# Kernel tuning notes

Hardware: AMD Instinct MI355X
Metric: run time of the kernel (lower is better)

Reference implementation:

```python
import jax, jax.numpy as jnp
import numpy as np

N_NODES = 100000
N_EDGES = 1600000
N_KEEP = 1280000  # int(N_EDGES * (1 - thr_a)), thr_a = 0.2
F_IN = 128
F_OUT = 128


def setup_inputs() -> dict:
    key = jax.random.key(0)
    ks = jax.random.split(key, 7)
    x = jax.random.normal(ks[0], (N_NODES, F_IN), dtype=jnp.float32)
    W = jax.random.normal(ks[1], (F_OUT, F_IN), dtype=jnp.float32) * (1.0 / np.sqrt(F_IN))
    bias = jax.random.normal(ks[2], (F_OUT,), dtype=jnp.float32)
    edge_src = jax.random.randint(ks[3], (N_EDGES,), 0, N_NODES, dtype=jnp.int32)
    edge_dst = jax.random.randint(ks[4], (N_EDGES,), 0, N_NODES, dtype=jnp.int32)
    edge_weight = jax.random.uniform(ks[5], (N_EDGES,), dtype=jnp.float32)
    idx_keep = jax.random.randint(ks[6], (N_KEEP,), 0, N_EDGES, dtype=jnp.int32)
    return {"x": x, "W": W, "bias": bias, "edge_src": edge_src,
            "edge_dst": edge_dst, "edge_weight": edge_weight, "idx_keep": idx_keep}


def reference(x, W, bias, edge_src, edge_dst, edge_weight, idx_keep):
    # Linear transform (pyg GCNConv lin has bias=False): h = x @ W.T  -> [N, F_out]
    h = jnp.einsum('nf,of->no', x, W)
    # Edge pruning: keep a random subset of edges (scheme_a='keep')
    src = edge_src[idx_keep]          # [M_keep]
    dst = edge_dst[idx_keep]          # [M_keep]
    ew = edge_weight[idx_keep]        # [M_keep]
    # propagate: message_j = h[src] * ew ; scatter-add into dst
    msg = h[src] * ew[:, None]        # [M_keep, F_out]
    out = jax.ops.segment_sum(msg, dst, num_segments=N_NODES)
    # GCNConv separate bias
    out = out + bias
    return out
```

## Files before the change

### kernel.cpp

```cpp
#include <hip/hip_runtime.h>

#define F 128
#define LDS_STRIDE 136
#define BUCKET 48

#define NPART 64
#define PCAP 22000
#define BIN_CAP 80
#define PA_CHUNK 2048
#define PB_CHUNK 1024
#define PB_CHUNKS 22

typedef __attribute__((ext_vector_type(8))) short short8;
typedef __attribute__((ext_vector_type(8))) unsigned short u16x8;
typedef __attribute__((ext_vector_type(4))) float floatx4;
typedef __attribute__((ext_vector_type(4))) float f32x4;

__device__ __forceinline__ unsigned short f32_to_bf16(float x) {
    unsigned u = __float_as_uint(x);
    unsigned r = u + 0x7FFFu + ((u >> 16) & 1u);
    return (unsigned short)(r >> 16);
}
__device__ __forceinline__ float bf16_to_f32(unsigned short h) {
    return __uint_as_float(((unsigned)h) << 16);
}

__global__ __launch_bounds__(256, 2) void gemm_mfma(const float4* __restrict__ x4,
                                                    const float4* __restrict__ W4,
                                                    unsigned short* __restrict__ h2,
                                                    int* __restrict__ zero_region,
                                                    int n_zero,
                                                    int n_nodes) {
    __shared__ short xs[128 * LDS_STRIDE];
    __shared__ short wls[128 * LDS_STRIDE];
    const int tid = threadIdx.x;
    const int node0 = blockIdx.x * 128;

    for (int i = blockIdx.x * 256 + tid; i < n_zero; i += gridDim.x * 256)
        zero_region[i] = 0;

    for (int i = tid; i < 128 * 32; i += 256) {
        int row = i >> 5, c4 = i & 31;
        float4 v = W4[i];
        ushort4 b;
        b.x = f32_to_bf16(v.x); b.y = f32_to_bf16(v.y);
        b.z = f32_to_bf16(v.z); b.w = f32_to_bf16(v.w);
        *(ushort4*)&wls[row * LDS_STRIDE + c4 * 4] = b;
    }
    for (int i = tid; i < 128 * 32; i += 256) {
        int row = i >> 5, c4 = i & 31;
        int n = node0 + row;
        f32x4 v = (n < n_nodes)
                      ? __builtin_nontemporal_load((const f32x4*)&x4[(size_t)n * 32 + c4])
                      : (f32x4){0.f, 0.f, 0.f, 0.f};
        ushort4 b;
        b.x = f32_to_bf16(v[0]); b.y = f32_to_bf16(v[1]);
        b.z = f32_to_bf16(v[2]); b.w = f32_to_bf16(v[3]);
        *(ushort4*)&xs[row * LDS_STRIDE + c4 * 4] = b;
    }
    __syncthreads();

    const int wave = tid >> 6, lane = tid & 63;
    const int row16 = lane & 15, quad = lane >> 4;
    const int wrow0 = wave * 32;

    floatx4 acc[2][8];
    #pragma unroll
    for (int r = 0; r < 2; ++r)
        #pragma unroll
        for (int c = 0; c < 8; ++c)
            acc[r][c] = (floatx4){0.f, 0.f, 0.f, 0.f};

    #pragma unroll
    for (int s = 0; s < 4; ++s) {
        const int koff = s * 32 + quad * 8;
        short8 a[2];
        #pragma unroll
        for (int r = 0; r < 2; ++r)
            a[r] = *(const short8*)&xs[(wrow0 + r * 16 + row16) * LDS_STRIDE + koff];
        #pragma unroll
        for (int c = 0; c < 8; ++c) {
            short8 b = *(const short8*)&wls[(c * 16 + row16) * LDS_STRIDE + koff];
            acc[0][c] = __builtin_amdgcn_mfma_f32_16x16x32_bf16(a[0], b, acc[0][c], 0, 0, 0);
            acc[1][c] = __builtin_amdgcn_mfma_f32_16x16x32_bf16(a[1], b, acc[1][c], 0, 0, 0);
        }
    }

    #pragma unroll
    for (int r = 0; r < 2; ++r) {
        #pragma unroll
        for (int reg = 0; reg < 4; ++reg) {
            int n = node0 + wrow0 + r * 16 + quad * 4 + reg;
            if (n < n_nodes) {
                #pragma unroll
                for (int c = 0; c < 8; ++c)
                    h2[(size_t)n * F + c * 16 + row16] = f32_to_bf16(acc[r][c][reg]);
            }
        }
    }
}

__global__ __launch_bounds__(256) void fill_partition(const int* __restrict__ idx_keep,
                                                      const int* __restrict__ edge_dst,
                                                      unsigned* __restrict__ pair_buf,
                                                      int* __restrict__ pair_cnt,
                                                      int m, int npp) {
    __shared__ unsigned bins[NPART][BIN_CAP];
    __shared__ int bcnt[NPART];
    __shared__ int bbase[NPART];
    const int tid = threadIdx.x;

    for (int i = tid; i < NPART; i += 256) bcnt[i] = 0;
    __syncthreads();

    const int e0 = blockIdx.x * PA_CHUNK;
    #pragma unroll
    for (int k = 0; k < PA_CHUNK / 256; ++k) {
        int e = e0 + k * 256 + tid;
        if (e < m) {
            int ke = idx_keep[e];
            int d = edge_dst[ke];
            int p = d / npp;
            int dl = d - p * npp;
            unsigned entry = ((unsigned)dl << 21) | (unsigned)ke;
            int pos = atomicAdd(&bcnt[p], 1);
            if (pos < BIN_CAP) {
                bins[p][pos] = entry;
            } else {
                int g = atomicAdd(&pair_cnt[p], 1);
                if (g < PCAP) pair_buf[(size_t)p * PCAP + g] = entry;
            }
        }
    }
    __syncthreads();

    for (int i = tid; i < NPART; i += 256) {
        int c = min(bcnt[i], BIN_CAP);
        bbase[i] = atomicAdd(&pair_cnt[i], c);
    }
    __syncthreads();

    const int wave = tid >> 6, lane = tid & 63;
    for (int b = wave; b < NPART; b += 4) {
        int c = min(bcnt[b], BIN_CAP);
        int base = bbase[b];
        for (int j = lane; j < c; j += 64)
            if (base + j < PCAP)
                pair_buf[(size_t)b * PCAP + base + j] = bins[b][j];
    }
}

__global__ __launch_bounds__(256) void fill_scatter(const unsigned* __restrict__ pair_buf,
                                                    const int* __restrict__ pair_cnt,
                                                    int* __restrict__ cnt,
                                                    int* __restrict__ perm,
                                                    int npp) {
    const int p = blockIdx.x % NPART;
    const int chunk = blockIdx.x / NPART;
    const int n = min(pair_cnt[p], PCAP);
    const int i0 = chunk * PB_CHUNK;
    if (i0 >= n) return;
    #pragma unroll
    for (int k = 0; k < PB_CHUNK / 256; ++k) {
        int i = i0 + k * 256 + threadIdx.x;
        if (i < n) {
            unsigned e = pair_buf[(size_t)p * PCAP + i];
            int ke = (int)(e & 0x1FFFFFu);
            int d = p * npp + (int)(e >> 21);
            int pos = atomicAdd(&cnt[d], 1);
            if (pos < BUCKET) perm[d * BUCKET + pos] = ke;
        }
    }
}

__global__ __launch_bounds__(256) void pull_nodes4(const u16x8* __restrict__ h8,
                                                   const int* __restrict__ edge_src,
                                                   const float* __restrict__ edge_weight,
                                                   const int* __restrict__ cnt,
                                                   const int* __restrict__ perm,
                                                   const float4* __restrict__ bias4,
                                                   float4* __restrict__ out4,
                                                   int n_nodes) {
    const int node = blockIdx.x * 4 + (threadIdx.x >> 6);
    const int lane = threadIdx.x & 63;
    if (node >= n_nodes) return;

    const int deg = min(cnt[node], BUCKET);
    const int eh = lane >> 4, fl = lane & 15;
    float acc[8];
    #pragma unroll
    for (int i = 0; i < 8; ++i) acc[i] = 0.0f;

    int s = 0; float w = 0.0f;
    if (lane < deg) {
        int ke = perm[node * BUCKET + lane];
        s = edge_src[ke];
        w = edge_weight[ke];
    }
    for (int j = 0; j < deg; j += 4) {
        int jj = j + eh;
        int take = (jj < deg) ? jj : j;
        int   sj = __shfl(s, take, 64);
        float wj = __shfl(w, take, 64);
        if (jj >= deg) wj = 0.0f;
        u16x8 hv = h8[(size_t)sj * 16 + fl];
        #pragma unroll
        for (int i = 0; i < 8; ++i)
            acc[i] += bf16_to_f32((unsigned short)hv[i]) * wj;
    }
    #pragma unroll
    for (int i = 0; i < 8; ++i) {
        acc[i] += __shfl_xor(acc[i], 16, 64);
        acc[i] += __shfl_xor(acc[i], 32, 64);
    }
    if (lane < 16) {
        float4 b0 = bias4[fl * 2], b1 = bias4[fl * 2 + 1];
        f32x4 o0 = {acc[0] + b0.x, acc[1] + b0.y, acc[2] + b0.z, acc[3] + b0.w};
        f32x4 o1 = {acc[4] + b1.x, acc[5] + b1.y, acc[6] + b1.z, acc[7] + b1.w};
        __builtin_nontemporal_store(o0, (f32x4*)&out4[(size_t)node * 32 + fl * 2]);
        __builtin_nontemporal_store(o1, (f32x4*)&out4[(size_t)node * 32 + fl * 2 + 1]);
    }
}

extern "C" void kernel_launch(void* const* d_in, const int* in_sizes, int n_in,
                              void* d_out, int out_size, void* d_ws, size_t ws_size,
                              hipStream_t stream) {
    const float* x           = (const float*)d_in[0];
    const float* W           = (const float*)d_in[1];
    const float* bias        = (const float*)d_in[2];
    const int*   edge_src    = (const int*)d_in[3];
    const int*   edge_dst    = (const int*)d_in[4];
    const float* edge_weight = (const float*)d_in[5];
    const int*   idx_keep    = (const int*)d_in[6];
    float* out = (float*)d_out;

    const int n_nodes = in_sizes[0] / F;
    const int m_keep  = in_sizes[6];
    const int npp = (n_nodes + NPART - 1) / NPART;

    char* ws = (char*)d_ws;
    unsigned short* h2 = (unsigned short*)ws;
    size_t off = (size_t)n_nodes * F * 2;
    int* cnt = (int*)(ws + off);          off += (size_t)n_nodes * 4;
    int* pair_cnt = (int*)(ws + off);     off += 1024;
    unsigned* pair_buf = (unsigned*)(ws + off); off += (size_t)NPART * PCAP * 4;
    int* perm = (int*)(ws + off);

    const int n_zero = n_nodes + 256;

    gemm_mfma<<<(n_nodes + 127) / 128, 256, 0, stream>>>(
        (const float4*)x, (const float4*)W, h2, cnt, n_zero, n_nodes);

    fill_partition<<<(m_keep + PA_CHUNK - 1) / PA_CHUNK, 256, 0, stream>>>(
        idx_keep, edge_dst, pair_buf, pair_cnt, m_keep, npp);

    fill_scatter<<<NPART * PB_CHUNKS, 256, 0, stream>>>(
        pair_buf, pair_cnt, cnt, perm, npp);

    pull_nodes4<<<(n_nodes + 3) / 4, 256, 0, stream>>>(
        (const u16x8*)h2, edge_src, edge_weight, cnt, perm,
        (const float4*)bias, (float4*)out, n_nodes);
}
```

Before: 271.8 us.

## Fuse GEMM and edge partition into one interleaved kernel launch

Merges the bf16 MFMA linear transform and the edge-partition binning into a single kernel. Blocks are interleaved so that five of every nine do GEMM tiles and four do partition chunks, letting the compute-bound and gather-bound work run concurrently and saving one launch. The pair_cnt counters are now zeroed with a separate memset, because partition atomics can no longer rely on the GEMM kernel having cleared them first. The partition path also loads idx_keep as int4 vectors and pads the LDS bin stride to 81 to reduce bank conflicts. The shared-memory union and mixed block roles may lower occupancy for the partition blocks.

```diff
diff --git a/kernel.cpp b/kernel.cpp
--- a/kernel.cpp
+++ b/kernel.cpp
@@ -7,6 +7,7 @@
 #define NPART 64
 #define PCAP 22000
 #define BIN_CAP 80
+#define BIN_STRIDE 81
 #define PA_CHUNK 2048
 #define PB_CHUNK 1024
 #define PB_CHUNKS 22
@@ -25,128 +26,143 @@
     return __uint_as_float(((unsigned)h) << 16);
 }
 
-__global__ __launch_bounds__(256, 2) void gemm_mfma(const float4* __restrict__ x4,
-                                                    const float4* __restrict__ W4,
-                                                    unsigned short* __restrict__ h2,
-                                                    int* __restrict__ zero_region,
-                                                    int n_zero,
-                                                    int n_nodes) {
-    __shared__ short xs[128 * LDS_STRIDE];
-    __shared__ short wls[128 * LDS_STRIDE];
+__global__ __launch_bounds__(256, 2) void gemm_and_partition(
+    const float4* __restrict__ x4, const float4* __restrict__ W4,
+    unsigned short* __restrict__ h2,
+    int* __restrict__ cnt, int n_nodes,
+    const int* __restrict__ idx_keep, const int* __restrict__ edge_dst,
+    unsigned* __restrict__ pair_buf, int* __restrict__ pair_cnt,
+    int m, int npp, int n_gemm_tiles, int n_part_chunks)
+{
+    __shared__ __align__(16) char smem[2 * 128 * LDS_STRIDE * 2];
     const int tid = threadIdx.x;
-    const int node0 = blockIdx.x * 128;
-
-    for (int i = blockIdx.x * 256 + tid; i < n_zero; i += gridDim.x * 256)
-        zero_region[i] = 0;
-
-    for (int i = tid; i < 128 * 32; i += 256) {
-        int row = i >> 5, c4 = i & 31;
-        float4 v = W4[i];
-        ushort4 b;
-        b.x = f32_to_bf16(v.x); b.y = f32_to_bf16(v.y);
-        b.z = f32_to_bf16(v.z); b.w = f32_to_bf16(v.w);
-        *(ushort4*)&wls[row * LDS_STRIDE + c4 * 4] = b;
-    }
-    for (int i = tid; i < 128 * 32; i += 256) {
-        int row = i >> 5, c4 = i & 31;
-        int n = node0 + row;
-        f32x4 v = (n < n_nodes)
-                      ? __builtin_nontemporal_load((const f32x4*)&x4[(size_t)n * 32 + c4])
-                      : (f32x4){0.f, 0.f, 0.f, 0.f};
-        ushort4 b;
-        b.x = f32_to_bf16(v[0]); b.y = f32_to_bf16(v[1]);
-        b.z = f32_to_bf16(v[2]); b.w = f32_to_bf16(v[3]);
-        *(ushort4*)&xs[row * LDS_STRIDE + c4 * 4] = b;
-    }
-    __syncthreads();
-
-    const int wave = tid >> 6, lane = tid & 63;
-    const int row16 = lane & 15, quad = lane >> 4;
-    const int wrow0 = wave * 32;
-
-    floatx4 acc[2][8];
-    #pragma unroll
-    for (int r = 0; r < 2; ++r)
-        #pragma unroll
-        for (int c = 0; c < 8; ++c)
-            acc[r][c] = (floatx4){0.f, 0.f, 0.f, 0.f};
-
-    #pragma unroll
-    for (int s = 0; s < 4; ++s) {
-        const int koff = s * 32 + quad * 8;
-        short8 a[2];
-        #pragma unroll
-        for (int r = 0; r < 2; ++r)
-            a[r] = *(const short8*)&xs[(wrow0 + r * 16 + row16) * LDS_STRIDE + koff];
-        #pragma unroll
-        for (int c = 0; c < 8; ++c) {
-            short8 b = *(const short8*)&wls[(c * 16 + row16) * LDS_STRIDE + koff];
-            acc[0][c] = __builtin_amdgcn_mfma_f32_16x16x32_bf16(a[0], b, acc[0][c], 0, 0, 0);
-            acc[1][c] = __builtin_amdgcn_mfma_f32_16x16x32_bf16(a[1], b, acc[1][c], 0, 0, 0);
-        }
-    }
-
-    #pragma unroll
-    for (int r = 0; r < 2; ++r) {
-        #pragma unroll
-        for (int reg = 0; reg < 4; ++reg) {
-            int n = node0 + wrow0 + r * 16 + quad * 4 + reg;
-            if (n < n_nodes) {
-                #pragma unroll
-                for (int c = 0; c < 8; ++c)
-                    h2[(size_t)n * F + c * 16 + row16] = f32_to_bf16(acc[r][c][reg]);
-            }
-        }
-    }
-}
-
-__global__ __launch_bounds__(256) void fill_partition(const int* __restrict__ idx_keep,
-                                                      const int* __restrict__ edge_dst,
-                                                      unsigned* __restrict__ pair_buf,
-                                                      int* __restrict__ pair_cnt,
-                                                      int m, int npp) {
-    __shared__ unsigned bins[NPART][BIN_CAP];
-    __shared__ int bcnt[NPART];
-    __shared__ int bbase[NPART];
-    const int tid = threadIdx.x;
-
-    for (int i = tid; i < NPART; i += 256) bcnt[i] = 0;
-    __syncthreads();
-
-    const int e0 = blockIdx.x * PA_CHUNK;
-    #pragma unroll
-    for (int k = 0; k < PA_CHUNK / 256; ++k) {
-        int e = e0 + k * 256 + tid;
-        if (e < m) {
-            int ke = idx_keep[e];
-            int d = edge_dst[ke];
-            int p = d / npp;
-            int dl = d - p * npp;
-            unsigned entry = ((unsigned)dl << 21) | (unsigned)ke;
-            int pos = atomicAdd(&bcnt[p], 1);
-            if (pos < BIN_CAP) {
-                bins[p][pos] = entry;
+    const int bid = blockIdx.x;
+
+    for (int i = bid * 256 + tid; i < n_nodes; i += gridDim.x * 256)
+        cnt[i] = 0;
+
+    const int r = bid % 9, c = bid / 9;
+
+    if (r < 5) {
+        const int tile = c * 5 + r;
+        if (tile >= n_gemm_tiles) return;
+        short* xs  = (short*)smem;
+        short* wls = xs + 128 * LDS_STRIDE;
+        const int node0 = tile * 128;
+
+        for (int i = tid; i < 128 * 32; i += 256) {
+            int row = i >> 5, c4 = i & 31;
+            float4 v = W4[i];
+            ushort4 b;
+            b.x = f32_to_bf16(v.x); b.y = f32_to_bf16(v.y);
+            b.z = f32_to_bf16(v.z); b.w = f32_to_bf16(v.w);
+            *(ushort4*)&wls[row * LDS_STRIDE + c4 * 4] = b;
+        }
+        for (int i = tid; i < 128 * 32; i += 256) {
+            int row = i >> 5, c4 = i & 31;
+            int n = node0 + row;
+            f32x4 v = (n < n_nodes)
+                          ? __builtin_nontemporal_load((const f32x4*)&x4[(size_t)n * 32 + c4])
+                          : (f32x4){0.f, 0.f, 0.f, 0.f};
+            ushort4 b;
+            b.x = f32_to_bf16(v[0]); b.y = f32_to_bf16(v[1]);
+            b.z = f32_to_bf16(v[2]); b.w = f32_to_bf16(v[3]);
+            *(ushort4*)&xs[row * LDS_STRIDE + c4 * 4] = b;
+        }
+        __syncthreads();
+
+        const int wave = tid >> 6, lane = tid & 63;
+        const int row16 = lane & 15, quad = lane >> 4;
+        const int wrow0 = wave * 32;
+
+        floatx4 acc[2][8];
+        #pragma unroll
+        for (int rr = 0; rr < 2; ++rr)
+            #pragma unroll
+            for (int cc = 0; cc < 8; ++cc)
+                acc[rr][cc] = (floatx4){0.f, 0.f, 0.f, 0.f};
+
+        #pragma unroll
+        for (int s = 0; s < 4; ++s) {
+            const int koff = s * 32 + quad * 8;
+            short8 a[2];
+            #pragma unroll
+            for (int rr = 0; rr < 2; ++rr)
+                a[rr] = *(const short8*)&xs[(wrow0 + rr * 16 + row16) * LDS_STRIDE + koff];
+            #pragma unroll
+            for (int cc = 0; cc < 8; ++cc) {
+                short8 b = *(const short8*)&wls[(cc * 16 + row16) * LDS_STRIDE + koff];
+                acc[0][cc] = __builtin_amdgcn_mfma_f32_16x16x32_bf16(a[0], b, acc[0][cc], 0, 0, 0);
+                acc[1][cc] = __builtin_amdgcn_mfma_f32_16x16x32_bf16(a[1], b, acc[1][cc], 0, 0, 0);
+            }
+        }
+
+        #pragma unroll
+        for (int rr = 0; rr < 2; ++rr) {
+            #pragma unroll
+            for (int reg = 0; reg < 4; ++reg) {
+                int n = node0 + wrow0 + rr * 16 + quad * 4 + reg;
+                if (n < n_nodes) {
+                    #pragma unroll
+                    for (int cc = 0; cc < 8; ++cc)
+                        h2[(size_t)n * F + cc * 16 + row16] = f32_to_bf16(acc[rr][cc][reg]);
+                }
+            }
+        }
+    } else {
+        const int chunk = c * 4 + (r - 5);
+        if (chunk >= n_part_chunks) return;
+        unsigned (*bins)[BIN_STRIDE] = (unsigned (*)[BIN_STRIDE])smem;
+        int* bcnt  = (int*)(smem + NPART * BIN_STRIDE * 4);
+        int* bbase = bcnt + NPART;
+
+        for (int i = tid; i < NPART; i += 256) bcnt[i] = 0;
+        __syncthreads();
+
+        const int e0 = chunk * PA_CHUNK;
+        #pragma unroll
+        for (int k = 0; k < 2; ++k) {
+            const int e_lin = e0 + (k * 256 + tid) * 4;
+            int kes[4]; int nv = 0;
+            if (e_lin + 3 < m) {
+                int4 kv = *(const int4*)&idx_keep[e_lin];
+                kes[0] = kv.x; kes[1] = kv.y; kes[2] = kv.z; kes[3] = kv.w; nv = 4;
             } else {
-                int g = atomicAdd(&pair_cnt[p], 1);
-                if (g < PCAP) pair_buf[(size_t)p * PCAP + g] = entry;
-            }
-        }
-    }
-    __syncthreads();
-
-    for (int i = tid; i < NPART; i += 256) {
-        int c = min(bcnt[i], BIN_CAP);
-        bbase[i] = atomicAdd(&pair_cnt[i], c);
-    }
-    __syncthreads();
-
-    const int wave = tid >> 6, lane = tid & 63;
-    for (int b = wave; b < NPART; b += 4) {
-        int c = min(bcnt[b], BIN_CAP);
-        int base = bbase[b];
-        for (int j = lane; j < c; j += 64)
-            if (base + j < PCAP)
-                pair_buf[(size_t)b * PCAP + base + j] = bins[b][j];
+                for (int q = 0; q < 4; ++q)
+                    if (e_lin + q < m) { kes[nv++] = idx_keep[e_lin + q]; }
+            }
+            int ds[4];
+            for (int q = 0; q < nv; ++q) ds[q] = edge_dst[kes[q]];
+            for (int q = 0; q < nv; ++q) {
+                int d = ds[q];
+                int p = d / npp;
+                int dl = d - p * npp;
+                unsigned entry = ((unsigned)dl << 21) | (unsigned)kes[q];
+                int pos = atomicAdd(&bcnt[p], 1);
+                if (pos < BIN_CAP) {
+                    bins[p][pos] = entry;
+                } else {
+                    int g = atomicAdd(&pair_cnt[p], 1);
+                    if (g < PCAP) pair_buf[(size_t)p * PCAP + g] = entry;
+                }
+            }
+        }
+        __syncthreads();
+
+        for (int i = tid; i < NPART; i += 256) {
+            int cc = min(bcnt[i], BIN_CAP);
+            bbase[i] = atomicAdd(&pair_cnt[i], cc);
+        }
+        __syncthreads();
+
+        const int wave = tid >> 6, lane = tid & 63;
+        for (int b = wave; b < NPART; b += 4) {
+            int cc = min(bcnt[b], BIN_CAP);
+            int base = bbase[b];
+            for (int j = lane; j < cc; j += 64)
+                if (base + j < PCAP)
+                    pair_buf[(size_t)b * PCAP + base + j] = bins[b][j];
+        }
     }
 }
 
@@ -246,13 +262,17 @@
     unsigned* pair_buf = (unsigned*)(ws + off); off += (size_t)NPART * PCAP * 4;
     int* perm = (int*)(ws + off);
 
-    const int n_zero = n_nodes + 256;
-
-    gemm_mfma<<<(n_nodes + 127) / 128, 256, 0, stream>>>(
-        (const float4*)x, (const float4*)W, h2, cnt, n_zero, n_nodes);
-
-    fill_partition<<<(m_keep + PA_CHUNK - 1) / PA_CHUNK, 256, 0, stream>>>(
-        idx_keep, edge_dst, pair_buf, pair_cnt, m_keep, npp);
+    const int n_gemm_tiles  = (n_nodes + 127) / 128;
+    const int n_part_chunks = (m_keep + PA_CHUNK - 1) / PA_CHUNK;
+    const int gens = max((n_gemm_tiles + 4) / 5, (n_part_chunks + 3) / 4);
+    const int grid = 9 * gens;
+
+    hipMemsetAsync(pair_cnt, 0, 1024, stream);
+
+    gemm_and_partition<<<grid, 256, 0, stream>>>(
+        (const float4*)x, (const float4*)W, h2, cnt, n_nodes,
+        idx_keep, edge_dst, pair_buf, pair_cnt,
+        m_keep, npp, n_gemm_tiles, n_part_chunks);
 
     fill_scatter<<<NPART * PB_CHUNKS, 256, 0, stream>>>(
         pair_buf, pair_cnt, cnt, perm, npp);
```

Measured after the change: 268.3 us. No clear change (-1.3%).
